# Kernel optimization log

Hardware: AMD Instinct MI355X
Metric: run time of the kernel (lower is better)

Reference implementation:

```python
import jax, jax.numpy as jnp
import numpy as np

K = 3  # dynamic kernel size


def _conv(x, w, b, pad):
    # x: [B,Cin,H,W], w: [Cout,Cin,kh,kw]
    y = jax.lax.conv_general_dilated(
        x, w, window_strides=(1, 1), padding=pad,
        dimension_numbers=("NCHW", "OIHW", "NCHW"))
    return y + b[None, :, None, None]


def setup_inputs() -> dict:
    key = jax.random.key(0)
    ks = jax.random.split(key, 9)
    B, C, H, W = 16, 256, 64, 64
    sc1 = 1.0 / np.sqrt(C * 9)
    sc3 = 1.0 / np.sqrt(C)
    return {
        "x":    jax.random.normal(ks[0], (B, C, H, W), jnp.float32),
        "kin":  jax.random.normal(ks[1], (B, C, H, W), jnp.float32),
        "w1":   jax.random.normal(ks[2], (C, C, 3, 3), jnp.float32) * sc1,
        "b1":   jax.random.normal(ks[3], (C,), jnp.float32) * 0.01,
        "w2":   jax.random.normal(ks[4], (C, C, 3, 3), jnp.float32) * sc1,
        "b2":   jax.random.normal(ks[5], (C,), jnp.float32) * 0.01,
        "w3":   jax.random.normal(ks[6], (K * K * C, C, 1, 1), jnp.float32) * sc3,
        "b3":   jax.random.normal(ks[7], (K * K * C,), jnp.float32) * 0.01,
        "bias": jax.random.normal(ks[8], (C,), jnp.float32) * 0.01,
    }


def reference(x, kin, w1, b1, w2, b2, w3, b3, bias):
    B, C, H, W = x.shape
    # tokernel: conv3x3 (valid) -> lrelu(0.1) -> conv3x3 -> lrelu -> global avg pool -> 1x1 conv
    h = jax.nn.leaky_relu(_conv(kin, w1, b1, "VALID"), 0.1)
    h = jax.nn.leaky_relu(_conv(h, w2, b2, "VALID"), 0.1)
    p = h.mean(axis=(2, 3))                                   # [B,C] adaptive avg pool 1x1
    kern = jnp.einsum("bc,oc->bo", p, w3.reshape(K * K * C, C)) + b3  # 1x1 conv
    kern = kern.reshape(B, C, 1, K, K)                        # per-sample depthwise weights

    pad = [(K // 2, K // 2)] * 2

    def dw(xi, wi):  # xi: [C,H,W], wi: [C,1,K,K]
        return jax.lax.conv_general_dilated(
            xi[None], wi, window_strides=(1, 1), padding=pad,
            dimension_numbers=("NCHW", "OIHW", "NCHW"),
            feature_group_count=C)[0]

    y = jax.vmap(dw)(x, kern)                                 # [B,C,H,W]
    return y + bias[None, :, None, None]
```

## Files before the change

kernel.cpp:

```cpp
#include <hip/hip_runtime.h>
#include <hip/hip_bf16.h>
#include <stdint.h>

#define CCH 256

typedef __attribute__((ext_vector_type(8))) short short8;
typedef __attribute__((ext_vector_type(4))) float f32x4;

__device__ __forceinline__ float lrelu(float v) { return v > 0.f ? v : 0.1f * v; }

__device__ __forceinline__ unsigned short f2bf(float f) {
    __hip_bfloat16 h = __float2bfloat16(f);
    return *reinterpret_cast<unsigned short*>(&h);
}

__device__ __forceinline__ void gl_lds16(const void* g, void* s) {
    __builtin_amdgcn_global_load_lds(
        (const __attribute__((address_space(1))) unsigned int*)(uintptr_t)g,
        (__attribute__((address_space(3))) unsigned int*)(unsigned int)(uintptr_t)s,
        16, 0, 0);
}

__device__ __forceinline__ void pipe_barrier() {
    asm volatile("" ::: "memory");
    __builtin_amdgcn_s_barrier();
    asm volatile("" ::: "memory");
}

__global__ __launch_bounds__(256)
void nhwc_k(const float* __restrict__ in, unsigned short* __restrict__ out)
{
    __shared__ float t[32][65];
    const int tid = threadIdx.x;
    const int kc = blockIdx.x, y = blockIdx.y, b = blockIdx.z;
    const float* src = in + ((size_t)(b * 256 + kc * 32)) * 4096 + y * 64;
#pragma unroll
    for (int i = 0; i < 2; ++i) {
        int idx = tid + i * 256;
        int cl = idx >> 4, xg = idx & 15;
        float4 v = *(const float4*)(src + (size_t)cl * 4096 + xg * 4);
        t[cl][xg * 4 + 0] = v.x; t[cl][xg * 4 + 1] = v.y;
        t[cl][xg * 4 + 2] = v.z; t[cl][xg * 4 + 3] = v.w;
    }
    __syncthreads();
    const int x = tid >> 2, cg = tid & 3;
    union { unsigned short us[8]; uint4 v; } u;
#pragma unroll
    for (int j = 0; j < 8; ++j) u.us[j] = f2bf(t[cg * 8 + j][x]);
    unsigned short* dst = out + (((size_t)(b * 8 + kc) * 4096 + y * 64 + x) * 32 + cg * 8);
    *(uint4*)dst = u.v;
}

__global__ __launch_bounds__(256)
void wtr_k(const float* __restrict__ w1, const float* __restrict__ w2,
           unsigned short* __restrict__ o1, unsigned short* __restrict__ o2)
{
    const int ss = blockIdx.x;
    const int kc = ss / 9, t = ss - kc * 9;
    const float* w = blockIdx.y ? w2 : w1;
    unsigned short* o = blockIdx.y ? o2 : o1;
#pragma unroll
    for (int rep = 0; rep < 4; ++rep) {
        int slot = threadIdx.x + rep * 256;
        int f = slot >> 6, l = slot & 63;
        int co = f * 16 + (l & 15);
        int q  = l >> 4;
        union { unsigned short us[8]; uint4 v; } u;
#pragma unroll
        for (int uu = 0; uu < 8; ++uu)
            u.us[uu] = f2bf(w[((size_t)co * 256 + kc * 32 + q * 8 + uu) * 9 + t]);
        *(uint4*)(o + (size_t)ss * 8192 + slot * 8) = u.v;
    }
}

__global__ __launch_bounds__(256)
void zero_pool_k(float* __restrict__ p) { p[blockIdx.x * 256 + threadIdx.x] = 0.f; }

template<int POOL, int WIN, int WOUT>
__global__ __launch_bounds__(256, 2)
void convmm_k(const unsigned short* __restrict__ im, const unsigned short* __restrict__ wt,
              const float* __restrict__ bias, unsigned short* __restrict__ outp,
              float* __restrict__ pool)
{
    constexpr int HINPIX = WIN * WIN;
    constexpr int NVAL   = WOUT * WOUT;
    constexpr int NB = 16 * 512 + 8 * 512;
    __shared__ __align__(16) short Ls[3 * NB];

    const int tid  = threadIdx.x;
    const int wave = tid >> 6;
    const int lane = tid & 63;
    const int quad = lane >> 4;
    const int l15  = lane & 15;
    const int wm   = (wave & 1) * 128;
    const int wn   = (wave >> 1) * 64;
    const int nb0  = blockIdx.x * 128;
    const int b    = blockIdx.y;

    const unsigned short* abase = wt + (size_t)(wave * 4) * 512 + (size_t)lane * 8;
    size_t bofs[2];
#pragma unroll
    for (int h = 0; h < 2; ++h) {
        int nn = nb0 + (wave * 2 + h) * 16 + l15;
        if (nn > NVAL - 1) nn = NVAL - 1;
        int y = nn / WOUT, x = nn - y * WOUT;
        bofs[h] = ((size_t)(b * 8) * HINPIX + (size_t)y * WIN + x) * 32 + quad * 8;
    }

    f32x4 acc[8][4];
#pragma unroll
    for (int i = 0; i < 8; ++i)
#pragma unroll
        for (int j = 0; j < 4; ++j) { f32x4 z = {0.f, 0.f, 0.f, 0.f}; acc[i][j] = z; }

    auto stage = [&](int ss, short* buf) {
        const int kc = ss / 9, t = ss - kc * 9;
        const int ky = t / 3, kx = t - ky * 3;
        const size_t aoff = (size_t)ss * 8192;
        const size_t boff = ((size_t)kc * HINPIX + (size_t)ky * WIN + kx) * 32;
        short* bl = buf + 16 * 512;
#pragma unroll
        for (int h = 0; h < 4; ++h)
            gl_lds16(abase + aoff + h * 512, buf + (wave * 4 + h) * 512);
#pragma unroll
        for (int h = 0; h < 2; ++h)
            gl_lds16(im + bofs[h] + boff, bl + (wave * 2 + h) * 512);
    };

    auto compute = [&](const short* buf) {
        const short* ap = buf + (size_t)(wave & 1) * 8 * 512 + lane * 8;
        const short* bp = buf + 16 * 512 + (size_t)(wave >> 1) * 4 * 512 + lane * 8;
        short8 a[8], bfr[4];
#pragma unroll
        for (int i = 0; i < 8; ++i)
            a[i]  = *(const short8*)(ap + i * 512);
#pragma unroll
        for (int j = 0; j < 4; ++j)
            bfr[j] = *(const short8*)(bp + j * 512);
        __builtin_amdgcn_s_setprio(1);
#pragma unroll
        for (int i = 0; i < 8; ++i)
#pragma unroll
            for (int j = 0; j < 4; ++j)
                acc[i][j] = __builtin_amdgcn_mfma_f32_16x16x32_bf16(a[i], bfr[j], acc[i][j], 0, 0, 0);
        __builtin_amdgcn_s_setprio(0);
    };

    short* B0 = Ls;
    short* B1 = Ls + NB;
    short* B2 = Ls + 2 * NB;

    stage(0, B0);
    stage(1, B1);
    asm volatile("s_waitcnt vmcnt(6)" ::: "memory");
    pipe_barrier();

    short *c0 = B0, *c1 = B1, *c2 = B2;
    for (int s = 0; s < 70; ++s) {
        stage(s + 2, c2);
        compute(c0);
        asm volatile("s_waitcnt vmcnt(6)" ::: "memory");
        pipe_barrier();
        short* t = c0; c0 = c1; c1 = c2; c2 = t;
    }
    compute(c0);
    asm volatile("s_waitcnt vmcnt(0)" ::: "memory");
    pipe_barrier();
    compute(c1);

    const int co_l = wm + quad * 4;
    if (!POOL) {
#pragma unroll
        for (int i = 0; i < 8; ++i) {
            const int c0i = co_l + i * 16;
            float4 bv = *(const float4*)(bias + c0i);
            unsigned short* dstp = outp + ((size_t)(b * 8 + (c0i >> 5)) * NVAL) * 32 + (c0i & 31);
#pragma unroll
            for (int j = 0; j < 4; ++j) {
                int nn = nb0 + wn + j * 16 + l15;
                if (nn < NVAL) {
                    ushort4 pk = make_ushort4(
                        f2bf(lrelu(acc[i][j].x + bv.x)),
                        f2bf(lrelu(acc[i][j].y + bv.y)),
                        f2bf(lrelu(acc[i][j].z + bv.z)),
                        f2bf(lrelu(acc[i][j].w + bv.w)));
                    *(ushort4*)(dstp + (size_t)nn * 32) = pk;
                }
            }
        }
    } else {
#pragma unroll
        for (int i = 0; i < 8; ++i) {
            const int c0i = co_l + i * 16;
            float4 bv = *(const float4*)(bias + c0i);
            float s0 = 0.f, s1 = 0.f, s2 = 0.f, s3 = 0.f;
#pragma unroll
            for (int j = 0; j < 4; ++j) {
                int nn = nb0 + wn + j * 16 + l15;
                if (nn < NVAL) {
                    s0 += lrelu(acc[i][j].x + bv.x);
                    s1 += lrelu(acc[i][j].y + bv.y);
                    s2 += lrelu(acc[i][j].z + bv.z);
                    s3 += lrelu(acc[i][j].w + bv.w);
                }
            }
#pragma unroll
            for (int off = 1; off < 16; off <<= 1) {
                s0 += __shfl_xor(s0, off, 64);
                s1 += __shfl_xor(s1, off, 64);
                s2 += __shfl_xor(s2, off, 64);
                s3 += __shfl_xor(s3, off, 64);
            }
            if (l15 == 0) {
                float* pp = pool + b * 256 + c0i;
                atomicAdd(pp + 0, s0); atomicAdd(pp + 1, s1);
                atomicAdd(pp + 2, s2); atomicAdd(pp + 3, s3);
            }
        }
    }
}

__global__ __launch_bounds__(256)
void kern_gemm_k(const float* __restrict__ p, const float* __restrict__ w3,
                 const float* __restrict__ b3, float* __restrict__ kern)
{
    const int b = blockIdx.y;
    const int o = blockIdx.x * 256 + threadIdx.x;
    __shared__ float pv[CCH];
    pv[threadIdx.x] = p[b * CCH + threadIdx.x] * (1.f / 3600.f);
    __syncthreads();
    float acc = b3[o];
    const float* wr = w3 + (size_t)o * CCH;
#pragma unroll 4
    for (int c = 0; c < CCH; c += 4) {
        float4 wv = *(const float4*)(wr + c);
        acc += wv.x * pv[c] + wv.y * pv[c + 1] + wv.z * pv[c + 2] + wv.w * pv[c + 3];
    }
    kern[(size_t)b * (9 * CCH) + o] = acc;
}

__global__ __launch_bounds__(256)
void dw_k(const float* __restrict__ x, const float* __restrict__ kern,
          const float* __restrict__ bias, float* __restrict__ out)
{
    __shared__ float t[66 * 67];
    const int tid = threadIdx.x;
    const int bc = blockIdx.x;
    const int c = bc & (CCH - 1);
    const int b = bc >> 8;

#pragma unroll
    for (int i = 0; i < 18; ++i) {
        int idx = tid + i * 256;
        if (idx < 66 * 67) t[idx] = 0.f;
    }

    const float* kp = kern + (size_t)b * (9 * CCH) + c * 9;
    float k[9];
#pragma unroll
    for (int q = 0; q < 9; ++q) k[q] = kp[q];
    const float bs = bias[c];
    const float* xp = x + (size_t)bc * 4096;
    float* op = out + (size_t)bc * 4096;
    __syncthreads();

#pragma unroll
    for (int i = 0; i < 4; ++i) {
        int p4 = tid + i * 256;
        float4 v = *(const float4*)(xp + p4 * 4);
        int yy = p4 >> 4, xx = (p4 & 15) * 4;
        float* d = &t[(yy + 1) * 67 + 1 + xx];
        d[0] = v.x; d[1] = v.y; d[2] = v.z; d[3] = v.w;
    }
    __syncthreads();

#pragma unroll
    for (int i = 0; i < 4; ++i) {
        int p4 = tid + i * 256;
        int yy = p4 >> 4, xx = (p4 & 15) * 4;
        float r[3][6];
#pragma unroll
        for (int dy = 0; dy < 3; ++dy)
#pragma unroll
            for (int dx = 0; dx < 6; ++dx)
                r[dy][dx] = t[(yy + dy) * 67 + xx + dx];
        float4 o;
        float* ov = (float*)&o;
#pragma unroll
        for (int j = 0; j < 4; ++j) {
            float a = bs;
#pragma unroll
            for (int dy = 0; dy < 3; ++dy)
#pragma unroll
                for (int dx = 0; dx < 3; ++dx)
                    a += k[dy * 3 + dx] * r[dy][j + dx];
            ov[j] = a;
        }
        *(float4*)(op + p4 * 4) = o;
    }
}

extern "C" void kernel_launch(void* const* d_in, const int* in_sizes, int n_in,
                              void* d_out, int out_size, void* d_ws, size_t ws_size,
                              hipStream_t stream)
{
    const float* x    = (const float*)d_in[0];
    const float* kin  = (const float*)d_in[1];
    const float* w1   = (const float*)d_in[2];
    const float* b1   = (const float*)d_in[3];
    const float* w2   = (const float*)d_in[4];
    const float* b2   = (const float*)d_in[5];
    const float* w3   = (const float*)d_in[6];
    const float* b3   = (const float*)d_in[7];
    const float* bias = (const float*)d_in[8];

    unsigned short* imA = (unsigned short*)d_ws;
    unsigned short* h1  = imA + (size_t)16 * 8 * 4096 * 32;
    unsigned short* w1t = h1 + (size_t)16 * 8 * 3844 * 32 + 8192;
    unsigned short* w2t = w1t + (size_t)72 * 8192;
    float* pool = (float*)(w2t + (size_t)72 * 8192);
    float* kern = pool + 16 * 256;

    float* out = (float*)d_out;

    hipLaunchKernelGGL(zero_pool_k, dim3(16), dim3(256), 0, stream, pool);
    hipLaunchKernelGGL(nhwc_k, dim3(8, 64, 16), dim3(256), 0, stream, kin, imA);
    hipLaunchKernelGGL(wtr_k, dim3(72, 2), dim3(256), 0, stream, w1, w2, w1t, w2t);
    hipLaunchKernelGGL((convmm_k<0, 64, 62>), dim3(31, 16), dim3(256), 0, stream,
                       imA, w1t, b1, h1, (float*)nullptr);
    hipLaunchKernelGGL((convmm_k<1, 62, 60>), dim3(29, 16), dim3(256), 0, stream,
                       h1, w2t, b2, (unsigned short*)nullptr, pool);
    hipLaunchKernelGGL(kern_gemm_k, dim3(9, 16), dim3(256), 0, stream, pool, w3, b3, kern);
    hipLaunchKernelGGL(dw_k, dim3(16 * 256), dim3(256), 0, stream, x, kern, bias, out);
}
```

Baseline: 332.6 us.

## Load weight fragments directly into registers and shrink LDS staging to activations

The conv GEMM kernel no longer stages the weight (A) tiles through LDS. Each wave now loads its 8 A fragments straight from global memory into double-buffered registers one stage ahead, and only the im2col B tiles stay in the triple-buffered LDS ring. This cuts LDS footprint and LDS read traffic, and the loop is unrolled by two to alternate register buffers. In exchange, both wave pairs sharing an M half now fetch the same A data separately, register pressure rises, and the vmcnt waits now also cover the register loads. Separately, the depthwise kernel zeroes only the halo border of its LDS tile instead of the whole tile.

```diff
diff --git a/kernel.cpp b/kernel.cpp
--- a/kernel.cpp
+++ b/kernel.cpp
@@ -20,6 +20,8 @@
         (__attribute__((address_space(3))) unsigned int*)(unsigned int)(uintptr_t)s,
         16, 0, 0);
 }
+
+__device__ __forceinline__ void mem_fence_sched() { asm volatile("" ::: "memory"); }
 
 __device__ __forceinline__ void pipe_barrier() {
     asm volatile("" ::: "memory");
@@ -84,7 +86,7 @@
 {
     constexpr int HINPIX = WIN * WIN;
     constexpr int NVAL   = WOUT * WOUT;
-    constexpr int NB = 16 * 512 + 8 * 512;
+    constexpr int NB = 8 * 512;
     __shared__ __align__(16) short Ls[3 * NB];
 
     const int tid  = threadIdx.x;
@@ -97,7 +99,7 @@
     const int nb0  = blockIdx.x * 128;
     const int b    = blockIdx.y;
 
-    const unsigned short* abase = wt + (size_t)(wave * 4) * 512 + (size_t)lane * 8;
+    const unsigned short* abase = wt + (size_t)((wave & 1) * 8) * 512 + (size_t)lane * 8;
     size_t bofs[2];
 #pragma unroll
     for (int h = 0; h < 2; ++h) {
@@ -113,27 +115,27 @@
 #pragma unroll
         for (int j = 0; j < 4; ++j) { f32x4 z = {0.f, 0.f, 0.f, 0.f}; acc[i][j] = z; }
 
-    auto stage = [&](int ss, short* buf) {
+    short8 aA[8], aB[8];
+
+    auto loadA = [&](int ss, short8* ar) {
+        const unsigned short* ap = abase + (size_t)ss * 8192;
+#pragma unroll
+        for (int i = 0; i < 8; ++i)
+            ar[i] = *(const short8*)(ap + i * 512);
+    };
+
+    auto stageB = [&](int ss, short* buf) {
         const int kc = ss / 9, t = ss - kc * 9;
         const int ky = t / 3, kx = t - ky * 3;
-        const size_t aoff = (size_t)ss * 8192;
         const size_t boff = ((size_t)kc * HINPIX + (size_t)ky * WIN + kx) * 32;
-        short* bl = buf + 16 * 512;
-#pragma unroll
-        for (int h = 0; h < 4; ++h)
-            gl_lds16(abase + aoff + h * 512, buf + (wave * 4 + h) * 512);
 #pragma unroll
         for (int h = 0; h < 2; ++h)
-            gl_lds16(im + bofs[h] + boff, bl + (wave * 2 + h) * 512);
+            gl_lds16(im + bofs[h] + boff, buf + (wave * 2 + h) * 512);
     };
 
-    auto compute = [&](const short* buf) {
-        const short* ap = buf + (size_t)(wave & 1) * 8 * 512 + lane * 8;
-        const short* bp = buf + 16 * 512 + (size_t)(wave >> 1) * 4 * 512 + lane * 8;
-        short8 a[8], bfr[4];
-#pragma unroll
-        for (int i = 0; i < 8; ++i)
-            a[i]  = *(const short8*)(ap + i * 512);
+    auto compute = [&](const short* buf, const short8* ar) {
+        const short* bp = buf + (size_t)(wave >> 1) * 4 * 512 + lane * 8;
+        short8 bfr[4];
 #pragma unroll
         for (int j = 0; j < 4; ++j)
             bfr[j] = *(const short8*)(bp + j * 512);
@@ -142,31 +144,45 @@
         for (int i = 0; i < 8; ++i)
 #pragma unroll
             for (int j = 0; j < 4; ++j)
-                acc[i][j] = __builtin_amdgcn_mfma_f32_16x16x32_bf16(a[i], bfr[j], acc[i][j], 0, 0, 0);
+                acc[i][j] = __builtin_amdgcn_mfma_f32_16x16x32_bf16(ar[i], bfr[j], acc[i][j], 0, 0, 0);
         __builtin_amdgcn_s_setprio(0);
     };
 
-    short* B0 = Ls;
-    short* B1 = Ls + NB;
-    short* B2 = Ls + 2 * NB;
-
-    stage(0, B0);
-    stage(1, B1);
-    asm volatile("s_waitcnt vmcnt(6)" ::: "memory");
+    short* c0 = Ls;
+    short* c1 = Ls + NB;
+    short* c2 = Ls + 2 * NB;
+
+    loadA(0, aA);
+    mem_fence_sched();
+    stageB(0, c0);
+    stageB(1, c1);
+    asm volatile("s_waitcnt vmcnt(2)" ::: "memory");
     pipe_barrier();
 
-    short *c0 = B0, *c1 = B1, *c2 = B2;
-    for (int s = 0; s < 70; ++s) {
-        stage(s + 2, c2);
-        compute(c0);
-        asm volatile("s_waitcnt vmcnt(6)" ::: "memory");
+    for (int s = 0; s < 70; s += 2) {
+        loadA(s + 1, aB);
+        mem_fence_sched();
+        stageB(s + 2, c2);
+        mem_fence_sched();
+        compute(c0, aA);
+        asm volatile("s_waitcnt vmcnt(2)" ::: "memory");
         pipe_barrier();
-        short* t = c0; c0 = c1; c1 = c2; c2 = t;
-    }
-    compute(c0);
+        { short* t = c0; c0 = c1; c1 = c2; c2 = t; }
+        loadA(s + 2, aA);
+        mem_fence_sched();
+        stageB(s + 3, c2);
+        mem_fence_sched();
+        compute(c0, aB);
+        asm volatile("s_waitcnt vmcnt(2)" ::: "memory");
+        pipe_barrier();
+        { short* t = c0; c0 = c1; c1 = c2; c2 = t; }
+    }
+    loadA(71, aB);
+    mem_fence_sched();
+    compute(c0, aA);
     asm volatile("s_waitcnt vmcnt(0)" ::: "memory");
     pipe_barrier();
-    compute(c1);
+    compute(c1, aB);
 
     const int co_l = wm + quad * 4;
     if (!POOL) {
@@ -249,10 +265,10 @@
     const int c = bc & (CCH - 1);
     const int b = bc >> 8;
 
-#pragma unroll
-    for (int i = 0; i < 18; ++i) {
-        int idx = tid + i * 256;
-        if (idx < 66 * 67) t[idx] = 0.f;
+    if (tid < 67) { t[tid] = 0.f; t[65 * 67 + tid] = 0.f; }
+    if (tid >= 128 && tid < 192) {
+        int r = tid - 127;
+        t[r * 67] = 0.f; t[r * 67 + 65] = 0.f;
     }
 
     const float* kp = kern + (size_t)b * (9 * CCH) + c * 9;
```

After: 345.4 us. 1.04x slower.

## Enlarge conv GEMM tile to 256x256, four-stage LDS ring, register double-buffering

Applied to the files above, without the earlier changes.

The implicit-GEMM conv kernel moves to 512-thread blocks that each cover 256 output pixels instead of 128. That halves the grid and the per-CU re-fetch of weight tiles from global memory. The LDS ring grows to four stages, and LDS fragment reads are double-buffered in registers so the reads for the next step overlap the MFMAs of the current one. The depthwise kernel now zeroes only the halo border of its shared tile instead of the whole array. In exchange, the conv blocks use a much larger LDS footprint and more registers, and the tail-block waste on the N dimension changes.

```diff
diff --git a/kernel.cpp b/kernel.cpp
--- a/kernel.cpp
+++ b/kernel.cpp
@@ -20,6 +20,8 @@
         (__attribute__((address_space(3))) unsigned int*)(unsigned int)(uintptr_t)s,
         16, 0, 0);
 }
+
+__device__ __forceinline__ void mem_fence_sched() { asm volatile("" ::: "memory"); }
 
 __device__ __forceinline__ void pipe_barrier() {
     asm volatile("" ::: "memory");
@@ -77,15 +79,15 @@
 void zero_pool_k(float* __restrict__ p) { p[blockIdx.x * 256 + threadIdx.x] = 0.f; }
 
 template<int POOL, int WIN, int WOUT>
-__global__ __launch_bounds__(256, 2)
+__global__ __launch_bounds__(512, 1)
 void convmm_k(const unsigned short* __restrict__ im, const unsigned short* __restrict__ wt,
               const float* __restrict__ bias, unsigned short* __restrict__ outp,
               float* __restrict__ pool)
 {
     constexpr int HINPIX = WIN * WIN;
     constexpr int NVAL   = WOUT * WOUT;
-    constexpr int NB = 16 * 512 + 8 * 512;
-    __shared__ __align__(16) short Ls[3 * NB];
+    constexpr int NB = (16 + 16) * 512;
+    __shared__ __align__(16) short Ls[4 * NB];
 
     const int tid  = threadIdx.x;
     const int wave = tid >> 6;
@@ -94,10 +96,10 @@
     const int l15  = lane & 15;
     const int wm   = (wave & 1) * 128;
     const int wn   = (wave >> 1) * 64;
-    const int nb0  = blockIdx.x * 128;
+    const int nb0  = blockIdx.x * 256;
     const int b    = blockIdx.y;
 
-    const unsigned short* abase = wt + (size_t)(wave * 4) * 512 + (size_t)lane * 8;
+    const unsigned short* abase = wt + (size_t)(wave * 2) * 512 + (size_t)lane * 8;
     size_t bofs[2];
 #pragma unroll
     for (int h = 0; h < 2; ++h) {
@@ -120,53 +122,75 @@
         const size_t boff = ((size_t)kc * HINPIX + (size_t)ky * WIN + kx) * 32;
         short* bl = buf + 16 * 512;
 #pragma unroll
-        for (int h = 0; h < 4; ++h)
-            gl_lds16(abase + aoff + h * 512, buf + (wave * 4 + h) * 512);
+        for (int h = 0; h < 2; ++h)
+            gl_lds16(abase + aoff + h * 512, buf + (wave * 2 + h) * 512);
 #pragma unroll
         for (int h = 0; h < 2; ++h)
             gl_lds16(im + bofs[h] + boff, bl + (wave * 2 + h) * 512);
     };
 
-    auto compute = [&](const short* buf) {
+    auto readFrags = [&](const short* buf, short8 (&ar)[8], short8 (&br)[4]) {
         const short* ap = buf + (size_t)(wave & 1) * 8 * 512 + lane * 8;
         const short* bp = buf + 16 * 512 + (size_t)(wave >> 1) * 4 * 512 + lane * 8;
-        short8 a[8], bfr[4];
+#pragma unroll
+        for (int i = 0; i < 8; ++i) ar[i] = *(const short8*)(ap + i * 512);
+#pragma unroll
+        for (int j = 0; j < 4; ++j) br[j] = *(const short8*)(bp + j * 512);
+    };
+
+    auto compute = [&](const short8 (&ar)[8], const short8 (&br)[4]) {
+        __builtin_amdgcn_s_setprio(1);
 #pragma unroll
         for (int i = 0; i < 8; ++i)
-            a[i]  = *(const short8*)(ap + i * 512);
-#pragma unroll
-        for (int j = 0; j < 4; ++j)
-            bfr[j] = *(const short8*)(bp + j * 512);
-        __builtin_amdgcn_s_setprio(1);
-#pragma unroll
-        for (int i = 0; i < 8; ++i)
 #pragma unroll
             for (int j = 0; j < 4; ++j)
-                acc[i][j] = __builtin_amdgcn_mfma_f32_16x16x32_bf16(a[i], bfr[j], acc[i][j], 0, 0, 0);
+                acc[i][j] = __builtin_amdgcn_mfma_f32_16x16x32_bf16(ar[i], br[j], acc[i][j], 0, 0, 0);
         __builtin_amdgcn_s_setprio(0);
     };
 
-    short* B0 = Ls;
-    short* B1 = Ls + NB;
-    short* B2 = Ls + 2 * NB;
-
-    stage(0, B0);
-    stage(1, B1);
-    asm volatile("s_waitcnt vmcnt(6)" ::: "memory");
+    short* c0 = Ls;
+    short* c1 = Ls + NB;
+    short* c2 = Ls + 2 * NB;
+    short* c3 = Ls + 3 * NB;
+    short8 RA0[8], RB0[4], RA1[8], RB1[4];
+
+    stage(0, c0);
+    stage(1, c1);
+    stage(2, c2);
+    asm volatile("s_waitcnt vmcnt(4)" ::: "memory");
     pipe_barrier();
-
-    short *c0 = B0, *c1 = B1, *c2 = B2;
-    for (int s = 0; s < 70; ++s) {
-        stage(s + 2, c2);
-        compute(c0);
-        asm volatile("s_waitcnt vmcnt(6)" ::: "memory");
+    readFrags(c0, RA0, RB0);
+
+    for (int s = 0; s < 68; s += 2) {
+        readFrags(c1, RA1, RB1);
+        stage(s + 3, c3);
+        mem_fence_sched();
+        compute(RA0, RB0);
+        asm volatile("s_waitcnt vmcnt(4)" ::: "memory");
         pipe_barrier();
-        short* t = c0; c0 = c1; c1 = c2; c2 = t;
-    }
-    compute(c0);
+        { short* t = c0; c0 = c1; c1 = c2; c2 = c3; c3 = t; }
+        readFrags(c1, RA0, RB0);
+        stage(s + 4, c3);
+        mem_fence_sched();
+        compute(RA1, RB1);
+        asm volatile("s_waitcnt vmcnt(4)" ::: "memory");
+        pipe_barrier();
+        { short* t = c0; c0 = c1; c1 = c2; c2 = c3; c3 = t; }
+    }
+    readFrags(c1, RA1, RB1);
+    stage(71, c3);
+    mem_fence_sched();
+    compute(RA0, RB0);
+    asm volatile("s_waitcnt vmcnt(4)" ::: "memory");
+    pipe_barrier();
+    { short* t = c0; c0 = c1; c1 = c2; c2 = c3; c3 = t; }
+    readFrags(c1, RA0, RB0);
+    compute(RA1, RB1);
     asm volatile("s_waitcnt vmcnt(0)" ::: "memory");
     pipe_barrier();
-    compute(c1);
+    readFrags(c2, RA1, RB1);
+    compute(RA0, RB0);
+    compute(RA1, RB1);
 
     const int co_l = wm + quad * 4;
     if (!POOL) {
@@ -249,10 +273,10 @@
     const int c = bc & (CCH - 1);
     const int b = bc >> 8;
 
-#pragma unroll
-    for (int i = 0; i < 18; ++i) {
-        int idx = tid + i * 256;
-        if (idx < 66 * 67) t[idx] = 0.f;
+    if (tid < 67) { t[tid] = 0.f; t[65 * 67 + tid] = 0.f; }
+    if (tid >= 128 && tid < 192) {
+        int r = tid - 127;
+        t[r * 67] = 0.f; t[r * 67 + 65] = 0.f;
     }
 
     const float* kp = kern + (size_t)b * (9 * CCH) + c * 9;
@@ -326,9 +350,9 @@
     hipLaunchKernelGGL(zero_pool_k, dim3(16), dim3(256), 0, stream, pool);
     hipLaunchKernelGGL(nhwc_k, dim3(8, 64, 16), dim3(256), 0, stream, kin, imA);
     hipLaunchKernelGGL(wtr_k, dim3(72, 2), dim3(256), 0, stream, w1, w2, w1t, w2t);
-    hipLaunchKernelGGL((convmm_k<0, 64, 62>), dim3(31, 16), dim3(256), 0, stream,
+    hipLaunchKernelGGL((convmm_k<0, 64, 62>), dim3(16, 16), dim3(512), 0, stream,
                        imA, w1t, b1, h1, (float*)nullptr);
-    hipLaunchKernelGGL((convmm_k<1, 62, 60>), dim3(29, 16), dim3(256), 0, stream,
+    hipLaunchKernelGGL((convmm_k<1, 62, 60>), dim3(15, 16), dim3(512), 0, stream,
                        h1, w2t, b2, (unsigned short*)nullptr, pool);
     hipLaunchKernelGGL(kern_gemm_k, dim3(9, 16), dim3(256), 0, stream, pool, w3, b3, kern);
     hipLaunchKernelGGL(dw_k, dim3(16 * 256), dim3(256), 0, stream, x, kern, bias, out);
```

After: 335.4 us. Within noise of the previous version (+0.9%).
